# Kernel optimization log

Measured on AMD Instinct MI355X. Metric: run time of the kernel, lower is better.

Reference implementation:

```python
import jax, jax.numpy as jnp
import numpy as np

ITEM_NUMS = 100000
EMB_DIM = 128
HID_DIM = 128
N_ITEMS = 50000      # len(item_emb_idxes)
N_SESS = 50000       # rows of session_adj
N_TOTAL = N_SESS + N_ITEMS
NNZ_S = 500000
NNZ_A = 3200000
BATCH = 2048
N_SCORE = 50000


def setup_inputs() -> dict:
    key = jax.random.key(0)
    ks = jax.random.split(key, 12)
    return {
        "emb_table": jax.random.normal(ks[0], (ITEM_NUMS, EMB_DIM), jnp.float32),
        "W": jax.random.normal(ks[1], (EMB_DIM, HID_DIM), jnp.float32) * 0.01,
        "b": jax.random.normal(ks[2], (HID_DIM,), jnp.float32) * 0.01,
        "sess_vals": jax.random.uniform(ks[3], (NNZ_S,), jnp.float32),
        "A_vals": jax.random.uniform(ks[4], (NNZ_A,), jnp.float32),
        "batch_idxes": jax.random.randint(ks[5], (BATCH,), 0, N_TOTAL),
        "item_idxes": jax.random.randint(ks[6], (N_SCORE,), 0, N_TOTAL),
        "item_emb_idxes": jax.random.randint(ks[7], (N_ITEMS,), 0, ITEM_NUMS),
        "sess_rows": jax.random.randint(ks[8], (NNZ_S,), 0, N_SESS),
        "sess_cols": jax.random.randint(ks[9], (NNZ_S,), 0, N_ITEMS),
        "A_rows": jax.random.randint(ks[10], (NNZ_A,), 0, N_TOTAL),
        "A_cols": jax.random.randint(ks[11], (NNZ_A,), 0, N_TOTAL),
    }


def reference(emb_table, W, b, sess_vals, A_vals, batch_idxes, item_idxes,
              item_emb_idxes, sess_rows, sess_cols, A_rows, A_cols):
    # embedding gather: [N_ITEMS, EMB_DIM]
    x_item = emb_table[item_emb_idxes]
    # spmm(session_adj, x_item): [N_SESS, EMB_DIM]
    x_session = jax.ops.segment_sum(sess_vals[:, None] * x_item[sess_cols],
                                    sess_rows, num_segments=N_SESS)
    x = jnp.concatenate((x_session, x_item), axis=0)  # [N_TOTAL, EMB_DIM]
    # GCNconv: (x @ W) then spmm(A, .) + bias
    xw = x @ W                                         # [N_TOTAL, HID_DIM]
    h1 = jax.ops.segment_sum(A_vals[:, None] * xw[A_cols],
                             A_rows, num_segments=N_TOTAL) + b
    # score: [BATCH, N_SCORE]
    out = h1[batch_idxes] @ h1[item_idxes].T
    return out
```

## Files before the change

kernel.cpp:

```cpp
#include <hip/hip_runtime.h>

#define EMB 128
#define N_ITEMS 50000
#define N_SESS 50000
#define N_TOTAL 100000
#define NNZ_S 500000
#define NNZ_A 3200000
#define BATCH 2048
#define N_SCORE 50000

#define RPB 64
#define NB_A ((N_TOTAL + RPB - 1) / RPB)
#define NB_S ((N_SESS + RPB - 1) / RPB)
#define NBMAX 1600
#define EPT 8
#define EPB (256 * EPT)
#define NBLK_S ((NNZ_S + EPB - 1) / EPB)
#define NBLK_A ((NNZ_A + EPB - 1) / EPB)
#define CHUNK 4096

#define SB_X ((N_SCORE + 127) / 128)
#define SB_Y (BATCH / 128)
#define SB_TOT (SB_X * SB_Y)

typedef __attribute__((ext_vector_type(8))) short bf16x8;
typedef __attribute__((ext_vector_type(4))) float f32x4;

__device__ inline ushort f2bf(float f) {
    unsigned u = __float_as_uint(f);
    unsigned r = (u + 0x7fff + ((u >> 16) & 1)) >> 16;
    return (ushort)r;
}
__device__ inline float bflo(unsigned u) { return __uint_as_float(u << 16); }
__device__ inline float bfhi(unsigned u) { return __uint_as_float(u & 0xffff0000u); }

__global__ void k_mark2(const int* __restrict__ a, int na, const int* __restrict__ b, int nb_,
                        unsigned* __restrict__ bm) {
    int i = blockIdx.x * 256 + threadIdx.x;
    int r = -1;
    if (i < na) r = a[i];
    else if (i < na + nb_) r = b[i - na];
    if (r >= 0) atomicOr(&bm[r >> 5], 1u << (r & 31));
}

__global__ void k_gather_items_convW(const float* __restrict__ emb, const int* __restrict__ idx,
                                     ushort* __restrict__ xb_item,
                                     const float* __restrict__ W, ushort* __restrict__ Wt) {
    int blk = blockIdx.x;
    int tid = threadIdx.x;
    if (blk >= (N_ITEMS * 32) / 256) {
        int i = (blk - (N_ITEMS * 32) / 256) * 256 + tid;
        if (i < 128 * 128) {
            int n = i >> 7, k = i & 127;
            Wt[n * 128 + k] = f2bf(W[k * 128 + n]);
        }
        return;
    }
    int t = blk * 256 + tid;
    int i = t >> 5;
    int d = (t & 31) << 2;
    float4 v = *(const float4*)(emb + (long)idx[i] * EMB + d);
    uint2 o;
    o.x = (unsigned)f2bf(v.x) | ((unsigned)f2bf(v.y) << 16);
    o.y = (unsigned)f2bf(v.z) | ((unsigned)f2bf(v.w) << 16);
    *(uint2*)(xb_item + (long)i * EMB + d) = o;
}

__global__ __launch_bounds__(256) void k_hist2(const int* __restrict__ sRows, int* __restrict__ cntS,
                                               const int* __restrict__ aRows, int* __restrict__ cntA,
                                               const unsigned* __restrict__ bm) {
    __shared__ int h[NBMAX];
    int tid = threadIdx.x;
    const int* rows;
    int* cnt;
    const unsigned* filt;
    int nnz, nb;
    long b0;
    if (blockIdx.x < NBLK_S) {
        rows = sRows; cnt = cntS; filt = nullptr; nnz = NNZ_S; nb = NB_S;
        b0 = (long)blockIdx.x * EPB;
    } else {
        rows = aRows; cnt = cntA; filt = bm; nnz = NNZ_A; nb = NB_A;
        b0 = (long)(blockIdx.x - NBLK_S) * EPB;
    }
    for (int i = tid; i < nb; i += 256) h[i] = 0;
    __syncthreads();
#pragma unroll
    for (int j = 0; j < EPT; ++j) {
        long e = b0 + j * 256 + tid;
        if (e < nnz) {
            int r = rows[e];
            if (!filt || ((filt[r >> 5] >> (r & 31)) & 1))
                atomicAdd(&h[r >> 6], 1);
        }
    }
    __syncthreads();
    for (int i = tid; i < nb; i += 256) {
        int v = h[i];
        if (v) atomicAdd(&cnt[i], v);
    }
}

__global__ __launch_bounds__(1024) void k_scan2(const int* __restrict__ cntS, int* __restrict__ offS,
                                                const int* __restrict__ cntA, int* __restrict__ offA) {
    __shared__ int wsum[16];
    __shared__ int carry_s;
    const int* cnt = blockIdx.x ? cntA : cntS;
    int* off = blockIdx.x ? offA : offS;
    int n = blockIdx.x ? NB_A : NB_S;
    int tid = threadIdx.x, lane = tid & 63, wid = tid >> 6;
    if (tid == 0) carry_s = 0;
    __syncthreads();
    for (int base = 0; base < n; base += 1024) {
        int i = base + tid;
        int v = (i < n) ? cnt[i] : 0;
        int x = v;
#pragma unroll
        for (int s = 1; s < 64; s <<= 1) {
            int t = __shfl_up(x, s, 64);
            if (lane >= s) x += t;
        }
        if (lane == 63) wsum[wid] = x;
        __syncthreads();
        if (wid == 0) {
            int y = (lane < 16) ? wsum[lane] : 0;
#pragma unroll
            for (int s = 1; s < 16; s <<= 1) {
                int t = __shfl_up(y, s, 64);
                if (lane >= s) y += t;
            }
            if (lane < 16) wsum[lane] = y;
        }
        __syncthreads();
        int carry = carry_s;
        int wofs = (wid == 0) ? 0 : wsum[wid - 1];
        if (i < n) off[i] = carry + wofs + x - v;
        __syncthreads();
        if (tid == 0) carry_s = carry + wsum[15];
        __syncthreads();
    }
}

__global__ __launch_bounds__(256) void k_place2(const int* __restrict__ sRows, const int* __restrict__ sCols,
                                                const float* __restrict__ sVals, int* __restrict__ gtailS,
                                                int2* __restrict__ edgS,
                                                const int* __restrict__ aRows, const int* __restrict__ aCols,
                                                const float* __restrict__ aVals, int* __restrict__ gtailA,
                                                int2* __restrict__ edgA,
                                                const unsigned* __restrict__ bm) {
    __shared__ int h[NBMAX];
    __shared__ int base_s[NBMAX];
    int tid = threadIdx.x;
    const int *rows, *cols;
    const float* vals;
    int* gtail;
    int2* out;
    const unsigned* filt;
    int nnz, nb;
    long b0;
    if (blockIdx.x < NBLK_S) {
        rows = sRows; cols = sCols; vals = sVals; gtail = gtailS; out = edgS;
        filt = nullptr; nnz = NNZ_S; nb = NB_S;
        b0 = (long)blockIdx.x * EPB;
    } else {
        rows = aRows; cols = aCols; vals = aVals; gtail = gtailA; out = edgA;
        filt = bm; nnz = NNZ_A; nb = NB_A;
        b0 = (long)(blockIdx.x - NBLK_S) * EPB;
    }
    for (int i = tid; i < nb; i += 256) h[i] = 0;
    __syncthreads();
    int er[EPT], ec[EPT];
    float ev[EPT];
#pragma unroll
    for (int j = 0; j < EPT; ++j) {
        long e = b0 + j * 256 + tid;
        er[j] = -1;
        if (e < nnz) {
            int r = rows[e];
            if (!filt || ((filt[r >> 5] >> (r & 31)) & 1)) {
                er[j] = r;
                ec[j] = cols[e];
                ev[j] = vals[e];
                atomicAdd(&h[r >> 6], 1);
            }
        }
    }
    __syncthreads();
    for (int i = tid; i < nb; i += 256) {
        int v = h[i];
        if (v) base_s[i] = atomicAdd(&gtail[i], v);
        h[i] = 0;
    }
    __syncthreads();
#pragma unroll
    for (int j = 0; j < EPT; ++j) {
        if (er[j] >= 0) {
            int bk = er[j] >> 6;
            int loc = atomicAdd(&h[bk], 1);
            out[base_s[bk] + loc] = make_int2(((er[j] & 63) << 17) | ec[j], __float_as_int(ev[j]));
        }
    }
}

__global__ __launch_bounds__(512) void k_spmm_sorted(const int* __restrict__ gtail,
                                                     const int2* __restrict__ edges,
                                                     const ushort* __restrict__ src,
                                                     ushort* __restrict__ dst,
                                                     const float* __restrict__ bias,
                                                     int nrows,
                                                     const unsigned* __restrict__ bm) {
    __shared__ int2 se[CHUNK];
    __shared__ int hist[RPB], sofs[RPB], cur[RPB];
    int tid = threadIdx.x, lane = tid & 63, w = tid >> 6;
    int bk = blockIdx.x;
    int begin = bk ? gtail[bk - 1] : 0;
    int end = gtail[bk];

    float2 acc[8] = {};
    for (int cbase = begin; cbase < end; cbase += CHUNK) {
        int m = end - cbase;
        if (m > CHUNK) m = CHUNK;
        if (tid < RPB) hist[tid] = 0;
        __syncthreads();
        int2 er[CHUNK / 512];
#pragma unroll
        for (int j = 0; j < CHUNK / 512; ++j) {
            int idx = j * 512 + tid;
            if (idx < m) {
                er[j] = edges[cbase + idx];
                atomicAdd(&hist[er[j].x >> 17], 1);
            } else {
                er[j].x = -1;
            }
        }
        __syncthreads();
        if (w == 0) {
            int v = hist[lane];
            int x = v;
#pragma unroll
            for (int s = 1; s < 64; s <<= 1) {
                int t = __shfl_up(x, s, 64);
                if (lane >= s) x += t;
            }
            sofs[lane] = x - v;
            cur[lane] = x - v;
        }
        __syncthreads();
#pragma unroll
        for (int j = 0; j < CHUNK / 512; ++j) {
            if (er[j].x >= 0) {
                int lr = er[j].x >> 17;
                int p = atomicAdd(&cur[lr], 1);
                se[p] = er[j];
            }
        }
        __syncthreads();
#pragma unroll
        for (int i = 0; i < 8; ++i) {
            int lr = w * 8 + i;
            int e = sofs[lr];
            int s1 = e + hist[lr];
            for (; e + 4 <= s1; e += 4) {
                int2 e0 = se[e], e1 = se[e + 1], e2 = se[e + 2], e3 = se[e + 3];
                unsigned u0 = *(const unsigned*)(src + (long)(e0.x & 0x1FFFF) * EMB + lane * 2);
                unsigned u1 = *(const unsigned*)(src + (long)(e1.x & 0x1FFFF) * EMB + lane * 2);
                unsigned u2 = *(const unsigned*)(src + (long)(e2.x & 0x1FFFF) * EMB + lane * 2);
                unsigned u3 = *(const unsigned*)(src + (long)(e3.x & 0x1FFFF) * EMB + lane * 2);
                float v0 = __int_as_float(e0.y), v1 = __int_as_float(e1.y);
                float v2 = __int_as_float(e2.y), v3 = __int_as_float(e3.y);
                acc[i].x += v0 * bflo(u0) + v1 * bflo(u1) + v2 * bflo(u2) + v3 * bflo(u3);
                acc[i].y += v0 * bfhi(u0) + v1 * bfhi(u1) + v2 * bfhi(u2) + v3 * bfhi(u3);
            }
            for (; e < s1; ++e) {
                int2 e0 = se[e];
                unsigned u0 = *(const unsigned*)(src + (long)(e0.x & 0x1FFFF) * EMB + lane * 2);
                float v0 = __int_as_float(e0.y);
                acc[i].x += v0 * bflo(u0);
                acc[i].y += v0 * bfhi(u0);
            }
        }
        __syncthreads();
    }
#pragma unroll
    for (int i = 0; i < 8; ++i) {
        int r = bk * RPB + w * 8 + i;
        if (r < nrows && (!bm || ((bm[r >> 5] >> (r & 31)) & 1))) {
            float a = acc[i].x, c = acc[i].y;
            if (bias) {
                a += bias[lane * 2];
                c += bias[lane * 2 + 1];
            }
            unsigned o = (unsigned)f2bf(a) | ((unsigned)f2bf(c) << 16);
            *((unsigned*)(dst + (long)r * EMB) + lane) = o;
        }
    }
}

__global__ __launch_bounds__(256) void k_xw_mfma(const ushort* __restrict__ A,
                                                 const ushort* __restrict__ Wt,
                                                 ushort* __restrict__ xw, int nrows) {
    int wid = threadIdx.x >> 6;
    int lane = threadIdx.x & 63;
    int wm = wid >> 1, wn = wid & 1;
    long m0 = (long)blockIdx.x * 128 + wm * 64;
    int n0 = wn * 64;
    int r = lane & 15;
    int kg = lane >> 4;

    f32x4 acc[4][4] = {};
#pragma unroll
    for (int ks = 0; ks < 4; ++ks) {
        bf16x8 a[4], b[4];
#pragma unroll
        for (int mf = 0; mf < 4; ++mf) {
            long row = m0 + mf * 16 + r;
            if (row >= nrows) row = nrows - 1;
            a[mf] = *(const bf16x8*)(A + row * EMB + ks * 32 + kg * 8);
        }
#pragma unroll
        for (int nf = 0; nf < 4; ++nf) {
            int row = n0 + nf * 16 + r;
            b[nf] = *(const bf16x8*)(Wt + (long)row * EMB + ks * 32 + kg * 8);
        }
#pragma unroll
        for (int mf = 0; mf < 4; ++mf)
#pragma unroll
            for (int nf = 0; nf < 4; ++nf)
                acc[mf][nf] = __builtin_amdgcn_mfma_f32_16x16x32_bf16(a[mf], b[nf], acc[mf][nf], 0, 0, 0);
    }
#pragma unroll
    for (int mf = 0; mf < 4; ++mf) {
#pragma unroll
        for (int nf = 0; nf < 4; ++nf) {
            int col = n0 + nf * 16 + r;
#pragma unroll
            for (int j = 0; j < 4; ++j) {
                long row = m0 + mf * 16 + kg * 4 + j;
                if (row < nrows) xw[row * EMB + col] = f2bf(acc[mf][nf][j]);
            }
        }
    }
}

__global__ void k_gather_hbhi(const ushort* __restrict__ src,
                              const int* __restrict__ bidx, const int* __restrict__ iidx,
                              ushort* __restrict__ dst) {
    int t = blockIdx.x * blockDim.x + threadIdx.x;
    int i = t >> 4;
    int d = (t & 15) << 3;
    if (i >= BATCH + N_SCORE) return;
    int r = (i < BATCH) ? bidx[i] : iidx[i - BATCH];
    *(uint4*)(dst + (long)i * EMB + d) = *(const uint4*)(src + (long)r * EMB + d);
}

__global__ __launch_bounds__(256) void k_score_mfma(const ushort* __restrict__ A,
                                                    const ushort* __restrict__ B,
                                                    float* __restrict__ C) {
    const int q = SB_TOT / 8;
    int bid = blockIdx.x;
    int nb = (bid % 8) * q + bid / 8;
    int bx = nb / SB_Y;
    int by = nb % SB_Y;

    int wid = threadIdx.x >> 6;
    int lane = threadIdx.x & 63;
    int wm = wid >> 1, wn = wid & 1;
    long m0 = (long)by * 128 + wm * 64;
    long n0 = (long)bx * 128 + wn * 64;
    int r = lane & 15;
    int kg = lane >> 4;

    f32x4 acc[4][4] = {};
#pragma unroll
    for (int ks = 0; ks < 4; ++ks) {
        bf16x8 a[4], b[4];
#pragma unroll
        for (int mf = 0; mf < 4; ++mf) {
            long row = m0 + mf * 16 + r;
            a[mf] = *(const bf16x8*)(A + row * EMB + ks * 32 + kg * 8);
        }
#pragma unroll
        for (int nf = 0; nf < 4; ++nf) {
            long row = n0 + nf * 16 + r;
            if (row >= N_SCORE) row = N_SCORE - 1;
            b[nf] = *(const bf16x8*)(B + row * EMB + ks * 32 + kg * 8);
        }
#pragma unroll
        for (int mf = 0; mf < 4; ++mf)
#pragma unroll
            for (int nf = 0; nf < 4; ++nf)
                acc[mf][nf] = __builtin_amdgcn_mfma_f32_16x16x32_bf16(a[mf], b[nf], acc[mf][nf], 0, 0, 0);
    }
#pragma unroll
    for (int mf = 0; mf < 4; ++mf) {
#pragma unroll
        for (int nf = 0; nf < 4; ++nf) {
            long col = n0 + nf * 16 + r;
            if (col < N_SCORE) {
#pragma unroll
                for (int j = 0; j < 4; ++j) {
                    long row = m0 + mf * 16 + kg * 4 + j;
                    __builtin_nontemporal_store(acc[mf][nf][j], &C[row * N_SCORE + col]);
                }
            }
        }
    }
}

extern "C" void kernel_launch(void* const* d_in, const int* in_sizes, int n_in,
                              void* d_out, int out_size, void* d_ws, size_t ws_size,
                              hipStream_t stream) {
    const float* emb_table      = (const float*)d_in[0];
    const float* W              = (const float*)d_in[1];
    const float* b              = (const float*)d_in[2];
    const float* sess_vals      = (const float*)d_in[3];
    const float* A_vals         = (const float*)d_in[4];
    const int*   batch_idxes    = (const int*)d_in[5];
    const int*   item_idxes     = (const int*)d_in[6];
    const int*   item_emb_idxes = (const int*)d_in[7];
    const int*   sess_rows      = (const int*)d_in[8];
    const int*   sess_cols      = (const int*)d_in[9];
    const int*   A_rows         = (const int*)d_in[10];
    const int*   A_cols         = (const int*)d_in[11];
    float* out = (float*)d_out;

    char* base = (char*)d_ws;
    ushort*   xb_item = (ushort*)(base + 0);
    ushort*   xw      = (ushort*)(base + 12800000L);
    ushort*   h1      = (ushort*)(base + 38400000L);
    int2*     edgA    = (int2*)  (base + 64000000L);
    int2*     edgS    = (int2*)  (base + 89600000L);
    ushort*   Wt      = (ushort*)(base + 93600000L);
    ushort*   hb      = (ushort*)(base + 93632768L);
    ushort*   hi      = (ushort*)(base + 94157056L);
    unsigned* bm      = (unsigned*)(base + 106957056L);
    int*      cntBS   = (int*)   (base + 106969600L);
    int*      cntBA   = (int*)   (base + 106972728L);
    int*      gtailS  = (int*)   (base + 106978984L);
    int*      gtailA  = (int*)   (base + 106982112L);

    ushort* xw_item = xw + (long)N_SESS * EMB;

    hipMemsetAsync(bm, 0, 106978984L - 106957056L, stream);
    k_mark2<<<(BATCH + N_SCORE + 255) / 256, 256, 0, stream>>>(batch_idxes, BATCH,
                                                               item_idxes, N_SCORE, bm);
    k_hist2<<<NBLK_S + NBLK_A, 256, 0, stream>>>(sess_rows, cntBS, A_rows, cntBA, bm);
    k_scan2<<<2, 1024, 0, stream>>>(cntBS, gtailS, cntBA, gtailA);
    k_place2<<<NBLK_S + NBLK_A, 256, 0, stream>>>(sess_rows, sess_cols, sess_vals, gtailS, edgS,
                                                  A_rows, A_cols, A_vals, gtailA, edgA, bm);
    k_gather_items_convW<<<(N_ITEMS * 32) / 256 + 64, 256, 0, stream>>>(emb_table, item_emb_idxes,
                                                                        xb_item, W, Wt);
    k_xw_mfma<<<(N_ITEMS + 127) / 128, 256, 0, stream>>>(xb_item, Wt, xw_item, N_ITEMS);
    k_spmm_sorted<<<NB_S, 512, 0, stream>>>(gtailS, edgS, xw_item, xw, nullptr, N_SESS, nullptr);
    k_spmm_sorted<<<NB_A, 512, 0, stream>>>(gtailA, edgA, xw, h1, b, N_TOTAL, bm);
    k_gather_hbhi<<<((BATCH + N_SCORE) * 16 + 255) / 256, 256, 0, stream>>>(h1, batch_idxes,
                                                                            item_idxes, hb);
    k_score_mfma<<<SB_TOT, 256, 0, stream>>>(hb, hi, out);
}
```

Baseline: 441.8 us.

## Merge independent stages into shared launches and gather score rows inside the GEMM

The embedding gather and W conversion now run as extra blocks inside the histogram kernel. The x@W MFMA now runs as extra blocks inside the edge-placement kernel, so independent work overlaps in the same launch. The separate gather of batch and item rows into contiguous buffers is removed, and the score kernel reads h1 rows directly through the index arrays. This cuts three launches and one intermediate copy, at the cost of indirect loads in the score GEMM and larger shared-memory and register footprints for the merged kernels.

```diff
diff --git a/kernel.cpp b/kernel.cpp
--- a/kernel.cpp
+++ b/kernel.cpp
@@ -17,6 +17,8 @@
 #define EPB (256 * EPT)
 #define NBLK_S ((NNZ_S + EPB - 1) / EPB)
 #define NBLK_A ((NNZ_A + EPB - 1) / EPB)
+#define GATHER_BLKS ((N_ITEMS * 32) / 256)
+#define XW_BLKS ((N_ITEMS + 127) / 128)
 #define CHUNK 4096
 
 #define SB_X ((N_SCORE + 127) / 128)
@@ -43,61 +45,58 @@
     if (r >= 0) atomicOr(&bm[r >> 5], 1u << (r & 31));
 }
 
-__global__ void k_gather_items_convW(const float* __restrict__ emb, const int* __restrict__ idx,
-                                     ushort* __restrict__ xb_item,
-                                     const float* __restrict__ W, ushort* __restrict__ Wt) {
+__global__ __launch_bounds__(256) void k_mega1(const int* __restrict__ sRows, int* __restrict__ cntS,
+                                               const int* __restrict__ aRows, int* __restrict__ cntA,
+                                               const unsigned* __restrict__ bm,
+                                               const float* __restrict__ emb,
+                                               const int* __restrict__ emb_idx,
+                                               ushort* __restrict__ xb_item,
+                                               const float* __restrict__ W, ushort* __restrict__ Wt) {
+    __shared__ int h[NBMAX];
     int blk = blockIdx.x;
     int tid = threadIdx.x;
-    if (blk >= (N_ITEMS * 32) / 256) {
-        int i = (blk - (N_ITEMS * 32) / 256) * 256 + tid;
-        if (i < 128 * 128) {
-            int n = i >> 7, k = i & 127;
-            Wt[n * 128 + k] = f2bf(W[k * 128 + n]);
-        }
-        return;
-    }
-    int t = blk * 256 + tid;
-    int i = t >> 5;
-    int d = (t & 31) << 2;
-    float4 v = *(const float4*)(emb + (long)idx[i] * EMB + d);
-    uint2 o;
-    o.x = (unsigned)f2bf(v.x) | ((unsigned)f2bf(v.y) << 16);
-    o.y = (unsigned)f2bf(v.z) | ((unsigned)f2bf(v.w) << 16);
-    *(uint2*)(xb_item + (long)i * EMB + d) = o;
-}
-
-__global__ __launch_bounds__(256) void k_hist2(const int* __restrict__ sRows, int* __restrict__ cntS,
-                                               const int* __restrict__ aRows, int* __restrict__ cntA,
-                                               const unsigned* __restrict__ bm) {
-    __shared__ int h[NBMAX];
-    int tid = threadIdx.x;
-    const int* rows;
-    int* cnt;
-    const unsigned* filt;
-    int nnz, nb;
-    long b0;
-    if (blockIdx.x < NBLK_S) {
-        rows = sRows; cnt = cntS; filt = nullptr; nnz = NNZ_S; nb = NB_S;
-        b0 = (long)blockIdx.x * EPB;
+    if (blk < NBLK_S + NBLK_A) {
+        const int* rows;
+        int* cnt;
+        const unsigned* filt;
+        int nnz, nb;
+        long b0;
+        if (blk < NBLK_S) {
+            rows = sRows; cnt = cntS; filt = nullptr; nnz = NNZ_S; nb = NB_S;
+            b0 = (long)blk * EPB;
+        } else {
+            rows = aRows; cnt = cntA; filt = bm; nnz = NNZ_A; nb = NB_A;
+            b0 = (long)(blk - NBLK_S) * EPB;
+        }
+        for (int i = tid; i < nb; i += 256) h[i] = 0;
+        __syncthreads();
+#pragma unroll
+        for (int j = 0; j < EPT; ++j) {
+            long e = b0 + j * 256 + tid;
+            if (e < nnz) {
+                int r = rows[e];
+                if (!filt || ((filt[r >> 5] >> (r & 31)) & 1))
+                    atomicAdd(&h[r >> 6], 1);
+            }
+        }
+        __syncthreads();
+        for (int i = tid; i < nb; i += 256) {
+            int v = h[i];
+            if (v) atomicAdd(&cnt[i], v);
+        }
+    } else if (blk < NBLK_S + NBLK_A + GATHER_BLKS) {
+        int t = (blk - NBLK_S - NBLK_A) * 256 + tid;
+        int i = t >> 5;
+        int d = (t & 31) << 2;
+        float4 v = *(const float4*)(emb + (long)emb_idx[i] * EMB + d);
+        uint2 o;
+        o.x = (unsigned)f2bf(v.x) | ((unsigned)f2bf(v.y) << 16);
+        o.y = (unsigned)f2bf(v.z) | ((unsigned)f2bf(v.w) << 16);
+        *(uint2*)(xb_item + (long)i * EMB + d) = o;
     } else {
-        rows = aRows; cnt = cntA; filt = bm; nnz = NNZ_A; nb = NB_A;
-        b0 = (long)(blockIdx.x - NBLK_S) * EPB;
-    }
-    for (int i = tid; i < nb; i += 256) h[i] = 0;
-    __syncthreads();
-#pragma unroll
-    for (int j = 0; j < EPT; ++j) {
-        long e = b0 + j * 256 + tid;
-        if (e < nnz) {
-            int r = rows[e];
-            if (!filt || ((filt[r >> 5] >> (r & 31)) & 1))
-                atomicAdd(&h[r >> 6], 1);
-        }
-    }
-    __syncthreads();
-    for (int i = tid; i < nb; i += 256) {
-        int v = h[i];
-        if (v) atomicAdd(&cnt[i], v);
+        int i = (blk - NBLK_S - NBLK_A - GATHER_BLKS) * 256 + tid;
+        int n = i >> 7, k = i & 127;
+        Wt[n * 128 + k] = f2bf(W[k * 128 + n]);
     }
 }
 
@@ -141,63 +140,112 @@
     }
 }
 
-__global__ __launch_bounds__(256) void k_place2(const int* __restrict__ sRows, const int* __restrict__ sCols,
-                                                const float* __restrict__ sVals, int* __restrict__ gtailS,
-                                                int2* __restrict__ edgS,
-                                                const int* __restrict__ aRows, const int* __restrict__ aCols,
-                                                const float* __restrict__ aVals, int* __restrict__ gtailA,
-                                                int2* __restrict__ edgA,
-                                                const unsigned* __restrict__ bm) {
+__global__ __launch_bounds__(256) void k_mega2(const int* __restrict__ sRows, const int* __restrict__ sCols,
+                                               const float* __restrict__ sVals, int* __restrict__ gtailS,
+                                               int2* __restrict__ edgS,
+                                               const int* __restrict__ aRows, const int* __restrict__ aCols,
+                                               const float* __restrict__ aVals, int* __restrict__ gtailA,
+                                               int2* __restrict__ edgA,
+                                               const unsigned* __restrict__ bm,
+                                               const ushort* __restrict__ xb_item,
+                                               const ushort* __restrict__ Wt,
+                                               ushort* __restrict__ xw_item) {
     __shared__ int h[NBMAX];
     __shared__ int base_s[NBMAX];
+    int blk = blockIdx.x;
     int tid = threadIdx.x;
-    const int *rows, *cols;
-    const float* vals;
-    int* gtail;
-    int2* out;
-    const unsigned* filt;
-    int nnz, nb;
-    long b0;
-    if (blockIdx.x < NBLK_S) {
-        rows = sRows; cols = sCols; vals = sVals; gtail = gtailS; out = edgS;
-        filt = nullptr; nnz = NNZ_S; nb = NB_S;
-        b0 = (long)blockIdx.x * EPB;
+    if (blk < NBLK_S + NBLK_A) {
+        const int *rows, *cols;
+        const float* vals;
+        int* gtail;
+        int2* out;
+        const unsigned* filt;
+        int nnz, nb;
+        long b0;
+        if (blk < NBLK_S) {
+            rows = sRows; cols = sCols; vals = sVals; gtail = gtailS; out = edgS;
+            filt = nullptr; nnz = NNZ_S; nb = NB_S;
+            b0 = (long)blk * EPB;
+        } else {
+            rows = aRows; cols = aCols; vals = aVals; gtail = gtailA; out = edgA;
+            filt = bm; nnz = NNZ_A; nb = NB_A;
+            b0 = (long)(blk - NBLK_S) * EPB;
+        }
+        for (int i = tid; i < nb; i += 256) h[i] = 0;
+        __syncthreads();
+        int er[EPT], ec[EPT];
+        float ev[EPT];
+#pragma unroll
+        for (int j = 0; j < EPT; ++j) {
+            long e = b0 + j * 256 + tid;
+            er[j] = -1;
+            if (e < nnz) {
+                int r = rows[e];
+                if (!filt || ((filt[r >> 5] >> (r & 31)) & 1)) {
+                    er[j] = r;
+                    ec[j] = cols[e];
+                    ev[j] = vals[e];
+                    atomicAdd(&h[r >> 6], 1);
+                }
+            }
+        }
+        __syncthreads();
+        for (int i = tid; i < nb; i += 256) {
+            int v = h[i];
+            if (v) base_s[i] = atomicAdd(&gtail[i], v);
+            h[i] = 0;
+        }
+        __syncthreads();
+#pragma unroll
+        for (int j = 0; j < EPT; ++j) {
+            if (er[j] >= 0) {
+                int bk = er[j] >> 6;
+                int loc = atomicAdd(&h[bk], 1);
+                out[base_s[bk] + loc] = make_int2(((er[j] & 63) << 17) | ec[j], __float_as_int(ev[j]));
+            }
+        }
     } else {
-        rows = aRows; cols = aCols; vals = aVals; gtail = gtailA; out = edgA;
-        filt = bm; nnz = NNZ_A; nb = NB_A;
-        b0 = (long)(blockIdx.x - NBLK_S) * EPB;
-    }
-    for (int i = tid; i < nb; i += 256) h[i] = 0;
-    __syncthreads();
-    int er[EPT], ec[EPT];
-    float ev[EPT];
-#pragma unroll
-    for (int j = 0; j < EPT; ++j) {
-        long e = b0 + j * 256 + tid;
-        er[j] = -1;
-        if (e < nnz) {
-            int r = rows[e];
-            if (!filt || ((filt[r >> 5] >> (r & 31)) & 1)) {
-                er[j] = r;
-                ec[j] = cols[e];
-                ev[j] = vals[e];
-                atomicAdd(&h[r >> 6], 1);
-            }
-        }
-    }
-    __syncthreads();
-    for (int i = tid; i < nb; i += 256) {
-        int v = h[i];
-        if (v) base_s[i] = atomicAdd(&gtail[i], v);
-        h[i] = 0;
-    }
-    __syncthreads();
-#pragma unroll
-    for (int j = 0; j < EPT; ++j) {
-        if (er[j] >= 0) {
-            int bk = er[j] >> 6;
-            int loc = atomicAdd(&h[bk], 1);
-            out[base_s[bk] + loc] = make_int2(((er[j] & 63) << 17) | ec[j], __float_as_int(ev[j]));
+        int bid = blk - NBLK_S - NBLK_A;
+        int wid = tid >> 6;
+        int lane = tid & 63;
+        int wm = wid >> 1, wn = wid & 1;
+        long m0 = (long)bid * 128 + wm * 64;
+        int n0 = wn * 64;
+        int r = lane & 15;
+        int kg = lane >> 4;
+
+        f32x4 acc[4][4] = {};
+#pragma unroll
+        for (int ks = 0; ks < 4; ++ks) {
+            bf16x8 a[4], b[4];
+#pragma unroll
+            for (int mf = 0; mf < 4; ++mf) {
+                long row = m0 + mf * 16 + r;
+                if (row >= N_ITEMS) row = N_ITEMS - 1;
+                a[mf] = *(const bf16x8*)(xb_item + row * EMB + ks * 32 + kg * 8);
+            }
+#pragma unroll
+            for (int nf = 0; nf < 4; ++nf) {
+                int row = n0 + nf * 16 + r;
+                b[nf] = *(const bf16x8*)(Wt + (long)row * EMB + ks * 32 + kg * 8);
+            }
+#pragma unroll
+            for (int mf = 0; mf < 4; ++mf)
+#pragma unroll
+                for (int nf = 0; nf < 4; ++nf)
+                    acc[mf][nf] = __builtin_amdgcn_mfma_f32_16x16x32_bf16(a[mf], b[nf], acc[mf][nf], 0, 0, 0);
+        }
+#pragma unroll
+        for (int mf = 0; mf < 4; ++mf) {
+#pragma unroll
+            for (int nf = 0; nf < 4; ++nf) {
+                int col = n0 + nf * 16 + r;
+#pragma unroll
+                for (int j = 0; j < 4; ++j) {
+                    long row = m0 + mf * 16 + kg * 4 + j;
+                    if (row < N_ITEMS) xw_item[row * EMB + col] = f2bf(acc[mf][nf][j]);
+                }
+            }
         }
     }
 }
@@ -296,65 +344,9 @@
     }
 }
 
-__global__ __launch_bounds__(256) void k_xw_mfma(const ushort* __restrict__ A,
-                                                 const ushort* __restrict__ Wt,
-                                                 ushort* __restrict__ xw, int nrows) {
-    int wid = threadIdx.x >> 6;
-    int lane = threadIdx.x & 63;
-    int wm = wid >> 1, wn = wid & 1;
-    long m0 = (long)blockIdx.x * 128 + wm * 64;
-    int n0 = wn * 64;
-    int r = lane & 15;
-    int kg = lane >> 4;
-
-    f32x4 acc[4][4] = {};
-#pragma unroll
-    for (int ks = 0; ks < 4; ++ks) {
-        bf16x8 a[4], b[4];
-#pragma unroll
-        for (int mf = 0; mf < 4; ++mf) {
-            long row = m0 + mf * 16 + r;
-            if (row >= nrows) row = nrows - 1;
-            a[mf] = *(const bf16x8*)(A + row * EMB + ks * 32 + kg * 8);
-        }
-#pragma unroll
-        for (int nf = 0; nf < 4; ++nf) {
-            int row = n0 + nf * 16 + r;
-            b[nf] = *(const bf16x8*)(Wt + (long)row * EMB + ks * 32 + kg * 8);
-        }
-#pragma unroll
-        for (int mf = 0; mf < 4; ++mf)
-#pragma unroll
-            for (int nf = 0; nf < 4; ++nf)
-                acc[mf][nf] = __builtin_amdgcn_mfma_f32_16x16x32_bf16(a[mf], b[nf], acc[mf][nf], 0, 0, 0);
-    }
-#pragma unroll
-    for (int mf = 0; mf < 4; ++mf) {
-#pragma unroll
-        for (int nf = 0; nf < 4; ++nf) {
-            int col = n0 + nf * 16 + r;
-#pragma unroll
-            for (int j = 0; j < 4; ++j) {
-                long row = m0 + mf * 16 + kg * 4 + j;
-                if (row < nrows) xw[row * EMB + col] = f2bf(acc[mf][nf][j]);
-            }
-        }
-    }
-}
-
-__global__ void k_gather_hbhi(const ushort* __restrict__ src,
-                              const int* __restrict__ bidx, const int* __restrict__ iidx,
-                              ushort* __restrict__ dst) {
-    int t = blockIdx.x * blockDim.x + threadIdx.x;
-    int i = t >> 4;
-    int d = (t & 15) << 3;
-    if (i >= BATCH + N_SCORE) return;
-    int r = (i < BATCH) ? bidx[i] : iidx[i - BATCH];
-    *(uint4*)(dst + (long)i * EMB + d) = *(const uint4*)(src + (long)r * EMB + d);
-}
-
-__global__ __launch_bounds__(256) void k_score_mfma(const ushort* __restrict__ A,
-                                                    const ushort* __restrict__ B,
+__global__ __launch_bounds__(256) void k_score_mfma(const ushort* __restrict__ H,
+                                                    const int* __restrict__ bidx,
+                                                    const int* __restrict__ iidx,
                                                     float* __restrict__ C) {
     const int q = SB_TOT / 8;
     int bid = blockIdx.x;
@@ -370,21 +362,26 @@
     int r = lane & 15;
     int kg = lane >> 4;
 
+    long arow[4], brow[4];
+#pragma unroll
+    for (int mf = 0; mf < 4; ++mf) arow[mf] = bidx[m0 + mf * 16 + r];
+#pragma unroll
+    for (int nf = 0; nf < 4; ++nf) {
+        long row = n0 + nf * 16 + r;
+        if (row >= N_SCORE) row = N_SCORE - 1;
+        brow[nf] = iidx[row];
+    }
+
     f32x4 acc[4][4] = {};
 #pragma unroll
     for (int ks = 0; ks < 4; ++ks) {
         bf16x8 a[4], b[4];
 #pragma unroll
-        for (int mf = 0; mf < 4; ++mf) {
-            long row = m0 + mf * 16 + r;
-            a[mf] = *(const bf16x8*)(A + row * EMB + ks * 32 + kg * 8);
-        }
-#pragma unroll
-        for (int nf = 0; nf < 4; ++nf) {
-            long row = n0 + nf * 16 + r;
-            if (row >= N_SCORE) row = N_SCORE - 1;
-            b[nf] = *(const bf16x8*)(B + row * EMB + ks * 32 + kg * 8);
-        }
+        for (int mf = 0; mf < 4; ++mf)
+            a[mf] = *(const bf16x8*)(H + arow[mf] * EMB + ks * 32 + kg * 8);
+#pragma unroll
+        for (int nf = 0; nf < 4; ++nf)
+            b[nf] = *(const bf16x8*)(H + brow[nf] * EMB + ks * 32 + kg * 8);
 #pragma unroll
         for (int mf = 0; mf < 4; ++mf)
 #pragma unroll
@@ -431,8 +428,6 @@
     int2*     edgA    = (int2*)  (base + 64000000L);
     int2*     edgS    = (int2*)  (base + 89600000L);
     ushort*   Wt      = (ushort*)(base + 93600000L);
-    ushort*   hb      = (ushort*)(base + 93632768L);
-    ushort*   hi      = (ushort*)(base + 94157056L);
     unsigned* bm      = (unsigned*)(base + 106957056L);
     int*      cntBS   = (int*)   (base + 106969600L);
     int*      cntBA   = (int*)   (base + 106972728L);
@@ -444,16 +439,15 @@
     hipMemsetAsync(bm, 0, 106978984L - 106957056L, stream);
     k_mark2<<<(BATCH + N_SCORE + 255) / 256, 256, 0, stream>>>(batch_idxes, BATCH,
                                                                item_idxes, N_SCORE, bm);
-    k_hist2<<<NBLK_S + NBLK_A, 256, 0, stream>>>(sess_rows, cntBS, A_rows, cntBA, bm);
+    k_mega1<<<NBLK_S + NBLK_A + GATHER_BLKS + 64, 256, 0, stream>>>(
+        sess_rows, cntBS, A_rows, cntBA, bm,
+        emb_table, item_emb_idxes, xb_item, W, Wt);
     k_scan2<<<2, 1024, 0, stream>>>(cntBS, gtailS, cntBA, gtailA);
-    k_place2<<<NBLK_S + NBLK_A, 256, 0, stream>>>(sess_rows, sess_cols, sess_vals, gtailS, edgS,
-                                                  A_rows, A_cols, A_vals, gtailA, edgA, bm);
-    k_gather_items_convW<<<(N_ITEMS * 32) / 256 + 64, 256, 0, stream>>>(emb_table, item_emb_idxes,
-                                                                        xb_item, W, Wt);
-    k_xw_mfma<<<(N_ITEMS + 127) / 128, 256, 0, stream>>>(xb_item, Wt, xw_item, N_ITEMS);
+    k_mega2<<<NBLK_S + NBLK_A + XW_BLKS, 256, 0, stream>>>(
+        sess_rows, sess_cols, sess_vals, gtailS, edgS,
+        A_rows, A_cols, A_vals, gtailA, edgA, bm,
+        xb_item, Wt, xw_item);
     k_spmm_sorted<<<NB_S, 512, 0, stream>>>(gtailS, edgS, xw_item, xw, nullptr, N_SESS, nullptr);
     k_spmm_sorted<<<NB_A, 512, 0, stream>>>(gtailA, edgA, xw, h1, b, N_TOTAL, bm);
-    k_gather_hbhi<<<((BATCH + N_SCORE) * 16 + 255) / 256, 256, 0, stream>>>(h1, batch_idxes,
-                                                                            item_idxes, hb);
-    k_score_mfma<<<SB_TOT, 256, 0, stream>>>(hb, hi, out);
-}
+    k_score_mfma<<<SB_TOT, 256, 0, stream>>>(h1, batch_idxes, item_idxes, out);
+}
```

New measurement: 410.1 us. 1.08x faster.
